# Kernel tuning notes

Measured on AMD Instinct MI355X. Metric: run time of the kernel, lower is better.

Reference implementation:

```python
import jax, jax.numpy as jnp
import numpy as np

N = 4096
IN_F = 512
OUT_F = 256
HEADS = 4
HEAD_DIM = OUT_F // HEADS


def setup_inputs() -> dict:
    key = jax.random.key(0)
    k_feat, k_adj, k_w, k_a = jax.random.split(key, 4)
    features = jax.random.normal(k_feat, (N, IN_F), dtype=jnp.float32)
    adj_matrix = jax.random.uniform(k_adj, (N, N), dtype=jnp.float32)
    # xavier-uniform-ish init scaled small
    W = jax.random.normal(k_w, (OUT_F, IN_F), dtype=jnp.float32) * (1.0 / np.sqrt(IN_F))
    a = jax.random.normal(k_a, (HEADS, 2 * HEAD_DIM), dtype=jnp.float32) * 0.1
    bias = jnp.zeros((OUT_F,), dtype=jnp.float32)
    return {"features": features, "adj_matrix": adj_matrix, "W": W, "a": a, "bias": bias}


def reference(features, adj_matrix, W, a, bias):
    n = features.shape[0]
    h = features @ W.T                      # [N, OUT_F]
    hh = h.reshape(n, HEADS, HEAD_DIM)      # [N, H, D]
    # e[i,j,h] = leaky_relu(<h_i, a[:, :D]> + <h_j, a[:, D:]>) -- additive decomposition
    e_src = jnp.einsum('nhd,hd->nh', hh, a[:, :HEAD_DIM])   # [N, H]
    e_dst = jnp.einsum('nhd,hd->nh', hh, a[:, HEAD_DIM:])   # [N, H]
    e = e_src[:, None, :] + e_dst[None, :, :]               # [N, N, H]
    e = jnp.where(e >= 0, e, 0.2 * e)                       # leaky_relu(0.2)
    mask = adj_matrix[:, :, None] > 0.1                     # [N, N, 1]
    e = jnp.where(mask, e, -jnp.inf)
    attention = jax.nn.softmax(e, axis=1)                   # softmax over j
    attention = jnp.nan_to_num(attention, nan=0.0)          # fully-masked rows -> 0
    attention_mean = attention.mean(axis=2)                 # [N, N]
    h_out = attention_mean @ h + bias                       # [N, OUT_F]
    return h_out
```

## Files before the change

### kernel.cpp

```cpp
#include <hip/hip_runtime.h>
#include <math.h>

#define NN      4096
#define INF_    512
#define OUTF    256
#define NHEAD   4
#define HDIM    64
#define KSPLIT  8

typedef __attribute__((ext_vector_type(8))) short  short8x;
typedef __attribute__((ext_vector_type(4))) float  float4x;
typedef __attribute__((ext_vector_type(2))) float  float2x;

__device__ __forceinline__ unsigned short f2bf(float x) {
    union { float f; unsigned int u; } c; c.f = x;
    unsigned int r = (c.u + 0x7FFFu + ((c.u >> 16) & 1u)) >> 16;
    return (unsigned short)r;
}
__device__ __forceinline__ unsigned int cvtpk_bf16(float lo, float hi) {
    unsigned int r;
    asm("v_cvt_pk_bf16_f32 %0, %1, %2" : "=v"(r) : "v"(lo), "v"(hi));
    return r;
}
__device__ __forceinline__ float2x bf2up(unsigned int u) {
    union { unsigned int x; float f; } lo, hi;
    lo.x = u << 16; hi.x = u & 0xFFFF0000u;
    float2x r; r[0] = lo.f; r[1] = hi.f; return r;
}
__device__ __forceinline__ float2x max2(float2x a, float2x b) {
    float2x r; r[0] = fmaxf(a[0], b[0]); r[1] = fmaxf(a[1], b[1]); return r;
}

__global__ __launch_bounds__(256) void k_cast(const float* __restrict__ feat,
                                              const float* __restrict__ W,
                                              const float* __restrict__ bias,
                                              unsigned short* __restrict__ featb,
                                              unsigned short* __restrict__ Wb,
                                              float* __restrict__ out) {
    const int b = blockIdx.x;
    const int tid = threadIdx.x;
    if (b >= 2176) {
        int idx = (b - 2176) * 1024 + tid * 4;
        float4x bv = *(const float4x*)(bias + ((tid * 4) & 255));
        *(float4x*)(out + idx) = bv;
        return;
    }
    const float* src;
    unsigned short* dst;
    int idx;
    if (b < 2048) { src = feat; dst = featb; idx = b * 1024 + tid * 4; }
    else          { src = W;    dst = Wb;    idx = (b - 2048) * 1024 + tid * 4; }
    float4x v = *(const float4x*)(src + idx);
    ushort4 u;
    u.x = f2bf(v[0]); u.y = f2bf(v[1]); u.z = f2bf(v[2]); u.w = f2bf(v[3]);
    *(ushort4*)(dst + idx) = u;
}

__global__ __launch_bounds__(256) void k_hedge(const unsigned short* __restrict__ featb,
                                               const unsigned short* __restrict__ Wb,
                                               const float* __restrict__ a,
                                               unsigned short* __restrict__ hT,
                                               float* __restrict__ es,
                                               unsigned short* __restrict__ Bt,
                                               unsigned short* __restrict__ Dt) {
    __shared__ __align__(16) unsigned short lds_f[32 * 40];
    __shared__ __align__(16) unsigned short lds_w[256 * 40];
    const int tid  = threadIdx.x;
    const int w    = tid >> 6;
    const int lane = tid & 63;
    const int lidx = lane & 15;
    const int quad = lane >> 4;
    const int i0   = blockIdx.x * 32;
    const int srf  = tid >> 3;
    const int skf  = (tid & 7) * 4;
    const int srw  = tid >> 2;
    const int skw  = (tid & 3) * 8;

    float4x acc[2][4];
    #pragma unroll
    for (int p = 0; p < 2; ++p)
        #pragma unroll
        for (int q = 0; q < 4; ++q)
            acc[p][q] = (float4x){0.f, 0.f, 0.f, 0.f};

    for (int kt = 0; kt < INF_; kt += 32) {
        __syncthreads();
        *(ushort4*)&lds_f[srf * 40 + skf] = *(const ushort4*)&featb[(size_t)(i0 + srf) * INF_ + kt + skf];
        #pragma unroll
        for (int itr = 0; itr < 4; ++itr) {
            int n = itr * 64 + srw;
            *(ushort4*)&lds_w[n * 40 + skw]     = *(const ushort4*)&Wb[(size_t)n * INF_ + kt + skw];
            *(ushort4*)&lds_w[n * 40 + skw + 4] = *(const ushort4*)&Wb[(size_t)n * INF_ + kt + skw + 4];
        }
        __syncthreads();
        short8x af[2], bw[4];
        #pragma unroll
        for (int t = 0; t < 2; ++t)
            af[t] = *(const short8x*)&lds_f[(t * 16 + lidx) * 40 + quad * 8];
        #pragma unroll
        for (int t = 0; t < 4; ++t)
            bw[t] = *(const short8x*)&lds_w[(w * 64 + t * 16 + lidx) * 40 + quad * 8];
        #pragma unroll
        for (int it = 0; it < 2; ++it)
            #pragma unroll
            for (int nt = 0; nt < 4; ++nt)
                acc[it][nt] = __builtin_amdgcn_mfma_f32_16x16x32_bf16(
                    af[it], bw[nt], acc[it][nt], 0, 0, 0);
    }
    #pragma unroll
    for (int it = 0; it < 2; ++it)
        #pragma unroll
        for (int nt = 0; nt < 4; ++nt) {
            int col = w * 64 + nt * 16 + lidx;
            int m0r = i0 + it * 16 + quad * 4;
            uint2 u;
            u.x = cvtpk_bf16(acc[it][nt][0], acc[it][nt][1]);
            u.y = cvtpk_bf16(acc[it][nt][2], acc[it][nt][3]);
            *(uint2*)&hT[(size_t)col * NN + m0r] = u;
        }
    float asrc[4], adst[4];
    #pragma unroll
    for (int nt = 0; nt < 4; ++nt) {
        asrc[nt] = a[w * 2 * HDIM + nt * 16 + lidx];
        adst[nt] = a[w * 2 * HDIM + HDIM + nt * 16 + lidx];
    }
    #pragma unroll
    for (int it = 0; it < 2; ++it)
        #pragma unroll
        for (int r = 0; r < 4; ++r) {
            float s = 0.f, d = 0.f;
            #pragma unroll
            for (int nt = 0; nt < 4; ++nt) {
                s += acc[it][nt][r] * asrc[nt];
                d += acc[it][nt][r] * adst[nt];
            }
            #pragma unroll
            for (int off = 1; off < 16; off <<= 1) {
                s += __shfl_xor(s, off);
                d += __shfl_xor(d, off);
            }
            if (lidx == 0) {
                int row = i0 + it * 16 + quad * 4 + r;
                es[row * NHEAD + w] = s;
                Bt[row * NHEAD + w] = f2bf(__expf(d));
                Dt[row * NHEAD + w] = f2bf(__expf(0.2f * d));
            }
        }
}

__global__ __launch_bounds__(256) void k_attn(const float* __restrict__ adj,
                                              const float* __restrict__ es,
                                              const unsigned short* __restrict__ Bt,
                                              const unsigned short* __restrict__ Dt,
                                              unsigned short* __restrict__ attn) {
    __shared__ float red[4][4];
    __shared__ float cfs[4];
    const int tid = threadIdx.x;
    const int wv  = tid >> 6;
    const int lane = tid & 63;
    const int i = blockIdx.x;

    const float4x esv = ((const float4x*)es)[i];
    float2x A01, A23, C01, C23;
    A01[0] = __expf(esv[0]); A01[1] = __expf(esv[1]);
    A23[0] = __expf(esv[2]); A23[1] = __expf(esv[3]);
    C01[0] = __expf(0.2f * esv[0]); C01[1] = __expf(0.2f * esv[1]);
    C23[0] = __expf(0.2f * esv[2]); C23[1] = __expf(0.2f * esv[3]);

    const float4x* arow4 = (const float4x*)(adj + (size_t)i * NN);
    const uint4* B4 = (const uint4*)Bt;
    const uint4* D4 = (const uint4*)Dt;

    float2x m01[4][4], m23[4][4];
    float2x den01 = (float2x){0.f, 0.f};
    float2x den23 = (float2x){0.f, 0.f};
    #pragma unroll
    for (int t = 0; t < 4; ++t) {
        int jv = t * 256 + tid;
        float4x av = arow4[jv];
        uint4 bu0 = B4[jv * 2], bu1 = B4[jv * 2 + 1];
        uint4 du0 = D4[jv * 2], du1 = D4[jv * 2 + 1];
        unsigned int bwv[8] = {bu0.x, bu0.y, bu0.z, bu0.w, bu1.x, bu1.y, bu1.z, bu1.w};
        unsigned int dwv[8] = {du0.x, du0.y, du0.z, du0.w, du1.x, du1.y, du1.z, du1.w};
        #pragma unroll
        for (int u = 0; u < 4; ++u) {
            float2x b01 = bf2up(bwv[u * 2]);
            float2x b23 = bf2up(bwv[u * 2 + 1]);
            float2x d01 = bf2up(dwv[u * 2]);
            float2x d23 = bf2up(dwv[u * 2 + 1]);
            float mf = (av[u] > 0.1f) ? 1.f : 0.f;
            float2x mf2; mf2[0] = mf; mf2[1] = mf;
            m01[t][u] = mf2 * max2(A01 * b01, C01 * d01);
            m23[t][u] = mf2 * max2(A23 * b23, C23 * d23);
            den01 += m01[t][u];
            den23 += m23[t][u];
        }
    }
    float dh[4] = {den01[0], den01[1], den23[0], den23[1]};
    #pragma unroll
    for (int off = 1; off < 64; off <<= 1) {
        #pragma unroll
        for (int h = 0; h < 4; ++h)
            dh[h] += __shfl_xor(dh[h], off);
    }
    if (lane == 0) {
        #pragma unroll
        for (int h = 0; h < 4; ++h) red[wv][h] = dh[h];
    }
    __syncthreads();
    if (tid < 4)
        cfs[tid] = red[0][tid] + red[1][tid] + red[2][tid] + red[3][tid];
    __syncthreads();
    float sc[4];
    #pragma unroll
    for (int h = 0; h < 4; ++h) {
        float den = cfs[h];
        sc[h] = den > 0.f ? 0.25f / den : 0.f;
    }

    unsigned short* orow = attn + (size_t)i * NN;
    #pragma unroll
    for (int t = 0; t < 4; ++t) {
        int jv = t * 256 + tid;
        float pv[4];
        #pragma unroll
        for (int u = 0; u < 4; ++u) {
            pv[u] = sc[0] * m01[t][u][0] + sc[1] * m01[t][u][1]
                  + sc[2] * m23[t][u][0] + sc[3] * m23[t][u][1];
        }
        uint2 o;
        o.x = cvtpk_bf16(pv[0], pv[1]);
        o.y = cvtpk_bf16(pv[2], pv[3]);
        *(uint2*)&orow[jv * 4] = o;
    }
}

__global__ __launch_bounds__(256) void k_out_gemm(const unsigned short* __restrict__ attn,
                                                  const unsigned short* __restrict__ hT,
                                                  float* __restrict__ out) {
    __shared__ __align__(16) unsigned short lds_a[32 * 72];
    __shared__ __align__(16) unsigned short lds_h[256 * 72];
    const int tid  = threadIdx.x;
    const int w    = tid >> 6;
    const int lane = tid & 63;
    const int lidx = lane & 15;
    const int quad = lane >> 4;
    const int i0    = blockIdx.x * 32;
    const int kbase = blockIdx.y * (NN / KSPLIT);
    const int sr   = tid >> 3;
    const int sc   = (tid & 7) * 8;

    float4x acc[2][4];
    #pragma unroll
    for (int p = 0; p < 2; ++p)
        #pragma unroll
        for (int q = 0; q < 4; ++q)
            acc[p][q] = (float4x){0.f, 0.f, 0.f, 0.f};

    short8x pa;
    short8x ph[8];
    pa = *(const short8x*)&attn[(size_t)(i0 + sr) * NN + kbase + sc];
    #pragma unroll
    for (int p = 0; p < 8; ++p)
        ph[p] = *(const short8x*)&hT[(size_t)(p * 32 + sr) * NN + kbase + sc];

    const int KSTEPS = (NN / KSPLIT) / 64;
    for (int ks = 0; ks < KSTEPS; ++ks) {
        __syncthreads();
        *(short8x*)&lds_a[sr * 72 + sc] = pa;
        #pragma unroll
        for (int p = 0; p < 8; ++p)
            *(short8x*)&lds_h[(p * 32 + sr) * 72 + sc] = ph[p];
        __syncthreads();
        if (ks + 1 < KSTEPS) {
            const int ko = kbase + (ks + 1) * 64;
            pa = *(const short8x*)&attn[(size_t)(i0 + sr) * NN + ko + sc];
            #pragma unroll
            for (int p = 0; p < 8; ++p)
                ph[p] = *(const short8x*)&hT[(size_t)(p * 32 + sr) * NN + ko + sc];
        }
        #pragma unroll
        for (int kk = 0; kk < 2; ++kk) {
            short8x af[2], bfr[4];
            #pragma unroll
            for (int it = 0; it < 2; ++it)
                af[it]  = *(const short8x*)&lds_a[(it * 16 + lidx) * 72 + kk * 32 + quad * 8];
            #pragma unroll
            for (int nt = 0; nt < 4; ++nt)
                bfr[nt] = *(const short8x*)&lds_h[(w * 64 + nt * 16 + lidx) * 72 + kk * 32 + quad * 8];
            #pragma unroll
            for (int it = 0; it < 2; ++it)
                #pragma unroll
                for (int nt = 0; nt < 4; ++nt)
                    acc[it][nt] = __builtin_amdgcn_mfma_f32_16x16x32_bf16(
                        af[it], bfr[nt], acc[it][nt], 0, 0, 0);
        }
    }
    #pragma unroll
    for (int it = 0; it < 2; ++it)
        #pragma unroll
        for (int nt = 0; nt < 4; ++nt)
            #pragma unroll
            for (int rr = 0; rr < 4; ++rr) {
                int row = i0 + it * 16 + quad * 4 + rr;
                int col = w * 64 + nt * 16 + lidx;
                unsafeAtomicAdd(&out[(size_t)row * OUTF + col], acc[it][nt][rr]);
            }
}

extern "C" void kernel_launch(void* const* d_in, const int* in_sizes, int n_in,
                              void* d_out, int out_size, void* d_ws, size_t ws_size,
                              hipStream_t stream) {
    const float* feat = (const float*)d_in[0];
    const float* adj  = (const float*)d_in[1];
    const float* W    = (const float*)d_in[2];
    const float* a    = (const float*)d_in[3];
    const float* bias = (const float*)d_in[4];
    float* out = (float*)d_out;

    char* ws = (char*)d_ws;
    float*          es    = (float*)(ws + 0);
    unsigned short* Btb   = (unsigned short*)(ws + (64u << 10));
    unsigned short* Dtb   = (unsigned short*)(ws + (96u << 10));
    unsigned short* hT    = (unsigned short*)(ws + (256u << 10));
    unsigned short* attn  = (unsigned short*)(ws + (2560u << 10));
    unsigned short* featb = (unsigned short*)(ws + (2560u << 10));
    unsigned short* Wb    = (unsigned short*)(ws + (6656u << 10));

    k_cast      <<<3200,              256, 0, stream>>>(feat, W, bias, featb, Wb, out);
    k_hedge     <<<128,               256, 0, stream>>>(featb, Wb, a, hT, es, Btb, Dtb);
    k_attn      <<<NN,                256, 0, stream>>>(adj, es, Btb, Dtb, attn);
    k_out_gemm  <<<dim3(128, KSPLIT), 256, 0, stream>>>(attn, hT, out);
}
```

Before: 172.2 us.

## Fuse attention-probability computation into output GEMM, split denominator pass

The attention kernel now only computes per-row softmax denominators and stores scaled per-head coefficients. The output GEMM recomputes the bf16 attention probabilities on the fly from adj, Bt and Dt instead of reading a materialized 32MB bf16 attention matrix. This removes the attention write and re-read, but reads adj twice (once per kernel) and adds exp-free elementwise work inside the GEMM loop. KSPLIT is also halved to 4, which reduces atomic traffic and gives longer K loops per block.

```diff
diff --git a/kernel.cpp b/kernel.cpp
--- a/kernel.cpp
+++ b/kernel.cpp
@@ -6,7 +6,7 @@
 #define OUTF    256
 #define NHEAD   4
 #define HDIM    64
-#define KSPLIT  8
+#define KSPLIT  4
 
 typedef __attribute__((ext_vector_type(8))) short  short8x;
 typedef __attribute__((ext_vector_type(4))) float  float4x;
@@ -148,11 +148,11 @@
         }
 }
 
-__global__ __launch_bounds__(256) void k_attn(const float* __restrict__ adj,
-                                              const float* __restrict__ es,
-                                              const unsigned short* __restrict__ Bt,
-                                              const unsigned short* __restrict__ Dt,
-                                              unsigned short* __restrict__ attn) {
+__global__ __launch_bounds__(256) void k_den(const float* __restrict__ adj,
+                                             const float* __restrict__ es,
+                                             const unsigned short* __restrict__ Bt,
+                                             const unsigned short* __restrict__ Dt,
+                                             float* __restrict__ cden) {
     __shared__ float red[4][4];
     __shared__ float cfs[4];
     const int tid = threadIdx.x;
@@ -171,7 +171,6 @@
     const uint4* B4 = (const uint4*)Bt;
     const uint4* D4 = (const uint4*)Dt;
 
-    float2x m01[4][4], m23[4][4];
     float2x den01 = (float2x){0.f, 0.f};
     float2x den23 = (float2x){0.f, 0.f};
     #pragma unroll
@@ -190,10 +189,8 @@
             float2x d23 = bf2up(dwv[u * 2 + 1]);
             float mf = (av[u] > 0.1f) ? 1.f : 0.f;
             float2x mf2; mf2[0] = mf; mf2[1] = mf;
-            m01[t][u] = mf2 * max2(A01 * b01, C01 * d01);
-            m23[t][u] = mf2 * max2(A23 * b23, C23 * d23);
-            den01 += m01[t][u];
-            den23 += m23[t][u];
+            den01 += mf2 * max2(A01 * b01, C01 * d01);
+            den23 += mf2 * max2(A23 * b23, C23 * d23);
         }
     }
     float dh[4] = {den01[0], den01[1], den23[0], den23[1]};
@@ -211,34 +208,29 @@
     if (tid < 4)
         cfs[tid] = red[0][tid] + red[1][tid] + red[2][tid] + red[3][tid];
     __syncthreads();
-    float sc[4];
-    #pragma unroll
-    for (int h = 0; h < 4; ++h) {
-        float den = cfs[h];
-        sc[h] = den > 0.f ? 0.25f / den : 0.f;
-    }
-
-    unsigned short* orow = attn + (size_t)i * NN;
-    #pragma unroll
-    for (int t = 0; t < 4; ++t) {
-        int jv = t * 256 + tid;
-        float pv[4];
-        #pragma unroll
-        for (int u = 0; u < 4; ++u) {
-            pv[u] = sc[0] * m01[t][u][0] + sc[1] * m01[t][u][1]
-                  + sc[2] * m23[t][u][0] + sc[3] * m23[t][u][1];
-        }
-        uint2 o;
-        o.x = cvtpk_bf16(pv[0], pv[1]);
-        o.y = cvtpk_bf16(pv[2], pv[3]);
-        *(uint2*)&orow[jv * 4] = o;
-    }
-}
-
-__global__ __launch_bounds__(256) void k_out_gemm(const unsigned short* __restrict__ attn,
-                                                  const unsigned short* __restrict__ hT,
-                                                  float* __restrict__ out) {
-    __shared__ __align__(16) unsigned short lds_a[32 * 72];
+    if (tid == 0) {
+        float A[4] = {A01[0], A01[1], A23[0], A23[1]};
+        float C[4] = {C01[0], C01[1], C23[0], C23[1]};
+        float4x cA, cC;
+        #pragma unroll
+        for (int h = 0; h < 4; ++h) {
+            float den = cfs[h];
+            float sc = den > 0.f ? 0.25f / den : 0.f;
+            cA[h] = A[h] * sc;
+            cC[h] = C[h] * sc;
+        }
+        ((float4x*)cden)[i * 2]     = cA;
+        ((float4x*)cden)[i * 2 + 1] = cC;
+    }
+}
+
+__global__ __launch_bounds__(256) void k_fused(const float* __restrict__ adj,
+                                               const float* __restrict__ cden,
+                                               const unsigned short* __restrict__ Bt,
+                                               const unsigned short* __restrict__ Dt,
+                                               const unsigned short* __restrict__ hT,
+                                               float* __restrict__ out) {
+    __shared__ __align__(16) unsigned short lds_p[32 * 72];
     __shared__ __align__(16) unsigned short lds_h[256 * 72];
     const int tid  = threadIdx.x;
     const int w    = tid >> 6;
@@ -248,7 +240,16 @@
     const int i0    = blockIdx.x * 32;
     const int kbase = blockIdx.y * (NN / KSPLIT);
     const int sr   = tid >> 3;
-    const int sc   = (tid & 7) * 8;
+    const int sc8  = (tid & 7) * 8;
+
+    const float4x cAv = ((const float4x*)cden)[(i0 + sr) * 2];
+    const float4x cCv = ((const float4x*)cden)[(i0 + sr) * 2 + 1];
+    float2x cA01, cA23, cC01, cC23;
+    cA01[0] = cAv[0]; cA01[1] = cAv[1]; cA23[0] = cAv[2]; cA23[1] = cAv[3];
+    cC01[0] = cCv[0]; cC01[1] = cCv[1]; cC23[0] = cCv[2]; cC23[1] = cCv[3];
+
+    const uint4* B4 = (const uint4*)Bt;
+    const uint4* D4 = (const uint4*)Dt;
 
     float4x acc[2][4];
     #pragma unroll
@@ -257,34 +258,69 @@
         for (int q = 0; q < 4; ++q)
             acc[p][q] = (float4x){0.f, 0.f, 0.f, 0.f};
 
-    short8x pa;
-    short8x ph[8];
-    pa = *(const short8x*)&attn[(size_t)(i0 + sr) * NN + kbase + sc];
-    #pragma unroll
-    for (int p = 0; p < 8; ++p)
-        ph[p] = *(const short8x*)&hT[(size_t)(p * 32 + sr) * NN + kbase + sc];
+    short8x pb[8];
+    short8x pp;
+
+    auto COMPP = [&](int ks) {
+        const int jb = kbase + ks * 64 + sc8;
+        float4x a0 = *(const float4x*)&adj[(size_t)(i0 + sr) * NN + jb];
+        float4x a1 = *(const float4x*)&adj[(size_t)(i0 + sr) * NN + jb + 4];
+        uint4 bu0 = B4[jb >> 1], bu1 = B4[(jb >> 1) + 1];
+        uint4 bu2 = B4[(jb >> 1) + 2], bu3 = B4[(jb >> 1) + 3];
+        uint4 du0 = D4[jb >> 1], du1 = D4[(jb >> 1) + 1];
+        uint4 du2 = D4[(jb >> 1) + 2], du3 = D4[(jb >> 1) + 3];
+        unsigned int bw[16] = {bu0.x, bu0.y, bu0.z, bu0.w, bu1.x, bu1.y, bu1.z, bu1.w,
+                               bu2.x, bu2.y, bu2.z, bu2.w, bu3.x, bu3.y, bu3.z, bu3.w};
+        unsigned int dw[16] = {du0.x, du0.y, du0.z, du0.w, du1.x, du1.y, du1.z, du1.w,
+                               du2.x, du2.y, du2.z, du2.w, du3.x, du3.y, du3.z, du3.w};
+        float pv[8];
+        #pragma unroll
+        for (int jj = 0; jj < 8; ++jj) {
+            float2x b01 = bf2up(bw[jj * 2]);
+            float2x b23 = bf2up(bw[jj * 2 + 1]);
+            float2x d01 = bf2up(dw[jj * 2]);
+            float2x d23 = bf2up(dw[jj * 2 + 1]);
+            float2x t01 = max2(cA01 * b01, cC01 * d01);
+            float2x t23 = max2(cA23 * b23, cC23 * d23);
+            float av = (jj < 4) ? a0[jj] : a1[jj - 4];
+            float s = (t01[0] + t01[1]) + (t23[0] + t23[1]);
+            pv[jj] = (av > 0.1f) ? s : 0.f;
+        }
+        union { short8x s; unsigned int u[4]; } pk;
+        pk.u[0] = cvtpk_bf16(pv[0], pv[1]);
+        pk.u[1] = cvtpk_bf16(pv[2], pv[3]);
+        pk.u[2] = cvtpk_bf16(pv[4], pv[5]);
+        pk.u[3] = cvtpk_bf16(pv[6], pv[7]);
+        pp = pk.s;
+    };
+    auto LOADB = [&](int ks) {
+        const int ko = kbase + ks * 64;
+        #pragma unroll
+        for (int p = 0; p < 8; ++p)
+            pb[p] = *(const short8x*)&hT[(size_t)(p * 32 + sr) * NN + ko + sc8];
+    };
+
+    LOADB(0);
+    COMPP(0);
 
     const int KSTEPS = (NN / KSPLIT) / 64;
     for (int ks = 0; ks < KSTEPS; ++ks) {
         __syncthreads();
-        *(short8x*)&lds_a[sr * 72 + sc] = pa;
+        *(short8x*)&lds_p[sr * 72 + sc8] = pp;
         #pragma unroll
         for (int p = 0; p < 8; ++p)
-            *(short8x*)&lds_h[(p * 32 + sr) * 72 + sc] = ph[p];
+            *(short8x*)&lds_h[(p * 32 + sr) * 72 + sc8] = pb[p];
         __syncthreads();
         if (ks + 1 < KSTEPS) {
-            const int ko = kbase + (ks + 1) * 64;
-            pa = *(const short8x*)&attn[(size_t)(i0 + sr) * NN + ko + sc];
-            #pragma unroll
-            for (int p = 0; p < 8; ++p)
-                ph[p] = *(const short8x*)&hT[(size_t)(p * 32 + sr) * NN + ko + sc];
+            LOADB(ks + 1);
+            COMPP(ks + 1);
         }
         #pragma unroll
         for (int kk = 0; kk < 2; ++kk) {
             short8x af[2], bfr[4];
             #pragma unroll
             for (int it = 0; it < 2; ++it)
-                af[it]  = *(const short8x*)&lds_a[(it * 16 + lidx) * 72 + kk * 32 + quad * 8];
+                af[it]  = *(const short8x*)&lds_p[(it * 16 + lidx) * 72 + kk * 32 + quad * 8];
             #pragma unroll
             for (int nt = 0; nt < 4; ++nt)
                 bfr[nt] = *(const short8x*)&lds_h[(w * 64 + nt * 16 + lidx) * 72 + kk * 32 + quad * 8];
@@ -322,13 +358,13 @@
     float*          es    = (float*)(ws + 0);
     unsigned short* Btb   = (unsigned short*)(ws + (64u << 10));
     unsigned short* Dtb   = (unsigned short*)(ws + (96u << 10));
+    float*          cden  = (float*)(ws + (128u << 10));
     unsigned short* hT    = (unsigned short*)(ws + (256u << 10));
-    unsigned short* attn  = (unsigned short*)(ws + (2560u << 10));
     unsigned short* featb = (unsigned short*)(ws + (2560u << 10));
     unsigned short* Wb    = (unsigned short*)(ws + (6656u << 10));
 
-    k_cast      <<<3200,              256, 0, stream>>>(feat, W, bias, featb, Wb, out);
-    k_hedge     <<<128,               256, 0, stream>>>(featb, Wb, a, hT, es, Btb, Dtb);
-    k_attn      <<<NN,                256, 0, stream>>>(adj, es, Btb, Dtb, attn);
-    k_out_gemm  <<<dim3(128, KSPLIT), 256, 0, stream>>>(attn, hT, out);
-}
+    k_cast <<<3200,              256, 0, stream>>>(feat, W, bias, featb, Wb, out);
+    k_hedge<<<128,               256, 0, stream>>>(featb, Wb, a, hT, es, Btb, Dtb);
+    k_den  <<<NN,                256, 0, stream>>>(adj, es, Btb, Dtb, cden);
+    k_fused<<<dim3(128, KSPLIT), 256, 0, stream>>>(adj, cden, Btb, Dtb, hT, out);
+}
```

Result: slower. 177.2 us (+2.9%).

## Fuse fp32-to-bf16 cast and bias init into projection GEMM kernel

Applied to the files above, without the earlier changes.

Drops the separate cast kernel. The projection kernel now loads fp32 features and W directly, converts them to bf16 as it stages them into LDS, and writes the bias into the output rows it owns. The row tile shrinks from 32 to 16 and the K step grows from 32 to 64, so the grid doubles to 256 blocks. This removes one launch and the bf16 round trip through global memory. In exchange, each block re-reads and re-converts the whole fp32 W matrix, which adds L2 traffic.

```diff
diff --git a/kernel.cpp b/kernel.cpp
--- a/kernel.cpp
+++ b/kernel.cpp
@@ -31,93 +31,88 @@
     float2x r; r[0] = fmaxf(a[0], b[0]); r[1] = fmaxf(a[1], b[1]); return r;
 }
 
-__global__ __launch_bounds__(256) void k_cast(const float* __restrict__ feat,
-                                              const float* __restrict__ W,
-                                              const float* __restrict__ bias,
-                                              unsigned short* __restrict__ featb,
-                                              unsigned short* __restrict__ Wb,
-                                              float* __restrict__ out) {
-    const int b = blockIdx.x;
-    const int tid = threadIdx.x;
-    if (b >= 2176) {
-        int idx = (b - 2176) * 1024 + tid * 4;
-        float4x bv = *(const float4x*)(bias + ((tid * 4) & 255));
-        *(float4x*)(out + idx) = bv;
-        return;
-    }
-    const float* src;
-    unsigned short* dst;
-    int idx;
-    if (b < 2048) { src = feat; dst = featb; idx = b * 1024 + tid * 4; }
-    else          { src = W;    dst = Wb;    idx = (b - 2048) * 1024 + tid * 4; }
-    float4x v = *(const float4x*)(src + idx);
-    ushort4 u;
-    u.x = f2bf(v[0]); u.y = f2bf(v[1]); u.z = f2bf(v[2]); u.w = f2bf(v[3]);
-    *(ushort4*)(dst + idx) = u;
-}
-
-__global__ __launch_bounds__(256) void k_hedge(const unsigned short* __restrict__ featb,
-                                               const unsigned short* __restrict__ Wb,
+__global__ __launch_bounds__(256) void k_hedge(const float* __restrict__ feat,
+                                               const float* __restrict__ W,
                                                const float* __restrict__ a,
+                                               const float* __restrict__ bias,
                                                unsigned short* __restrict__ hT,
                                                float* __restrict__ es,
                                                unsigned short* __restrict__ Bt,
-                                               unsigned short* __restrict__ Dt) {
-    __shared__ __align__(16) unsigned short lds_f[32 * 40];
-    __shared__ __align__(16) unsigned short lds_w[256 * 40];
+                                               unsigned short* __restrict__ Dt,
+                                               float* __restrict__ out) {
+    __shared__ __align__(16) unsigned short lds_f[16 * 72];
+    __shared__ __align__(16) unsigned short lds_w[256 * 72];
     const int tid  = threadIdx.x;
     const int w    = tid >> 6;
     const int lane = tid & 63;
     const int lidx = lane & 15;
     const int quad = lane >> 4;
-    const int i0   = blockIdx.x * 32;
-    const int srf  = tid >> 3;
-    const int skf  = (tid & 7) * 4;
-    const int srw  = tid >> 2;
-    const int skw  = (tid & 3) * 8;
-
-    float4x acc[2][4];
-    #pragma unroll
-    for (int p = 0; p < 2; ++p)
-        #pragma unroll
-        for (int q = 0; q < 4; ++q)
-            acc[p][q] = (float4x){0.f, 0.f, 0.f, 0.f};
-
-    for (int kt = 0; kt < INF_; kt += 32) {
+    const int i0   = blockIdx.x * 16;
+
+    {
+        float4x bv = *(const float4x*)(bias + ((tid * 4) & 255));
+        float* ob = out + (size_t)i0 * OUTF;
+        #pragma unroll
+        for (int itr = 0; itr < 4; ++itr)
+            *(float4x*)(ob + itr * 1024 + tid * 4) = bv;
+    }
+
+    const int fr = tid >> 4;
+    const int fc = (tid & 15) * 4;
+    const int wr = tid >> 2;
+    const int wc = (tid & 3) * 16;
+
+    float4x acc[4];
+    #pragma unroll
+    for (int q = 0; q < 4; ++q)
+        acc[q] = (float4x){0.f, 0.f, 0.f, 0.f};
+
+    for (int kt = 0; kt < INF_; kt += 64) {
         __syncthreads();
-        *(ushort4*)&lds_f[srf * 40 + skf] = *(const ushort4*)&featb[(size_t)(i0 + srf) * INF_ + kt + skf];
-        #pragma unroll
-        for (int itr = 0; itr < 4; ++itr) {
-            int n = itr * 64 + srw;
-            *(ushort4*)&lds_w[n * 40 + skw]     = *(const ushort4*)&Wb[(size_t)n * INF_ + kt + skw];
-            *(ushort4*)&lds_w[n * 40 + skw + 4] = *(const ushort4*)&Wb[(size_t)n * INF_ + kt + skw + 4];
+        {
+            float4x v = *(const float4x*)&feat[(size_t)(i0 + fr) * INF_ + kt + fc];
+            uint2 u;
+            u.x = cvtpk_bf16(v[0], v[1]);
+            u.y = cvtpk_bf16(v[2], v[3]);
+            *(uint2*)&lds_f[fr * 72 + fc] = u;
+        }
+        #pragma unroll
+        for (int p = 0; p < 4; ++p) {
+            int row = p * 64 + wr;
+            const float* src = &W[(size_t)row * INF_ + kt + wc];
+            float4x v0 = *(const float4x*)(src);
+            float4x v1 = *(const float4x*)(src + 4);
+            float4x v2 = *(const float4x*)(src + 8);
+            float4x v3 = *(const float4x*)(src + 12);
+            union { short8x s; unsigned int u[4]; } p0, p1;
+            p0.u[0] = cvtpk_bf16(v0[0], v0[1]); p0.u[1] = cvtpk_bf16(v0[2], v0[3]);
+            p0.u[2] = cvtpk_bf16(v1[0], v1[1]); p0.u[3] = cvtpk_bf16(v1[2], v1[3]);
+            p1.u[0] = cvtpk_bf16(v2[0], v2[1]); p1.u[1] = cvtpk_bf16(v2[2], v2[3]);
+            p1.u[2] = cvtpk_bf16(v3[0], v3[1]); p1.u[3] = cvtpk_bf16(v3[2], v3[3]);
+            *(short8x*)&lds_w[row * 72 + wc]     = p0.s;
+            *(short8x*)&lds_w[row * 72 + wc + 8] = p1.s;
         }
         __syncthreads();
-        short8x af[2], bw[4];
-        #pragma unroll
-        for (int t = 0; t < 2; ++t)
-            af[t] = *(const short8x*)&lds_f[(t * 16 + lidx) * 40 + quad * 8];
-        #pragma unroll
-        for (int t = 0; t < 4; ++t)
-            bw[t] = *(const short8x*)&lds_w[(w * 64 + t * 16 + lidx) * 40 + quad * 8];
-        #pragma unroll
-        for (int it = 0; it < 2; ++it)
+        #pragma unroll
+        for (int kk = 0; kk < 2; ++kk) {
+            short8x af = *(const short8x*)&lds_f[lidx * 72 + kk * 32 + quad * 8];
+            short8x bw[4];
             #pragma unroll
             for (int nt = 0; nt < 4; ++nt)
-                acc[it][nt] = __builtin_amdgcn_mfma_f32_16x16x32_bf16(
-                    af[it], bw[nt], acc[it][nt], 0, 0, 0);
-    }
-    #pragma unroll
-    for (int it = 0; it < 2; ++it)
-        #pragma unroll
-        for (int nt = 0; nt < 4; ++nt) {
-            int col = w * 64 + nt * 16 + lidx;
-            int m0r = i0 + it * 16 + quad * 4;
-            uint2 u;
-            u.x = cvtpk_bf16(acc[it][nt][0], acc[it][nt][1]);
-            u.y = cvtpk_bf16(acc[it][nt][2], acc[it][nt][3]);
-            *(uint2*)&hT[(size_t)col * NN + m0r] = u;
-        }
+                bw[nt] = *(const short8x*)&lds_w[(w * 64 + nt * 16 + lidx) * 72 + kk * 32 + quad * 8];
+            #pragma unroll
+            for (int nt = 0; nt < 4; ++nt)
+                acc[nt] = __builtin_amdgcn_mfma_f32_16x16x32_bf16(af, bw[nt], acc[nt], 0, 0, 0);
+        }
+    }
+    #pragma unroll
+    for (int nt = 0; nt < 4; ++nt) {
+        int col = w * 64 + nt * 16 + lidx;
+        uint2 u;
+        u.x = cvtpk_bf16(acc[nt][0], acc[nt][1]);
+        u.y = cvtpk_bf16(acc[nt][2], acc[nt][3]);
+        *(uint2*)&hT[(size_t)col * NN + i0 + quad * 4] = u;
+    }
     float asrc[4], adst[4];
     #pragma unroll
     for (int nt = 0; nt < 4; ++nt) {
@@ -125,27 +120,25 @@
         adst[nt] = a[w * 2 * HDIM + HDIM + nt * 16 + lidx];
     }
     #pragma unroll
-    for (int it = 0; it < 2; ++it)
-        #pragma unroll
-        for (int r = 0; r < 4; ++r) {
-            float s = 0.f, d = 0.f;
-            #pragma unroll
-            for (int nt = 0; nt < 4; ++nt) {
-                s += acc[it][nt][r] * asrc[nt];
-                d += acc[it][nt][r] * adst[nt];
-            }
-            #pragma unroll
-            for (int off = 1; off < 16; off <<= 1) {
-                s += __shfl_xor(s, off);
-                d += __shfl_xor(d, off);
-            }
-            if (lidx == 0) {
-                int row = i0 + it * 16 + quad * 4 + r;
-                es[row * NHEAD + w] = s;
-                Bt[row * NHEAD + w] = f2bf(__expf(d));
-                Dt[row * NHEAD + w] = f2bf(__expf(0.2f * d));
-            }
-        }
+    for (int r = 0; r < 4; ++r) {
+        float s = 0.f, d = 0.f;
+        #pragma unroll
+        for (int nt = 0; nt < 4; ++nt) {
+            s += acc[nt][r] * asrc[nt];
+            d += acc[nt][r] * adst[nt];
+        }
+        #pragma unroll
+        for (int off = 1; off < 16; off <<= 1) {
+            s += __shfl_xor(s, off);
+            d += __shfl_xor(d, off);
+        }
+        if (lidx == 0) {
+            int row = i0 + quad * 4 + r;
+            es[row * NHEAD + w] = s;
+            Bt[row * NHEAD + w] = f2bf(__expf(d));
+            Dt[row * NHEAD + w] = f2bf(__expf(0.2f * d));
+        }
+    }
 }
 
 __global__ __launch_bounds__(256) void k_attn(const float* __restrict__ adj,
@@ -324,11 +317,8 @@
     unsigned short* Dtb   = (unsigned short*)(ws + (96u << 10));
     unsigned short* hT    = (unsigned short*)(ws + (256u << 10));
     unsigned short* attn  = (unsigned short*)(ws + (2560u << 10));
-    unsigned short* featb = (unsigned short*)(ws + (2560u << 10));
-    unsigned short* Wb    = (unsigned short*)(ws + (6656u << 10));
-
-    k_cast      <<<3200,              256, 0, stream>>>(feat, W, bias, featb, Wb, out);
-    k_hedge     <<<128,               256, 0, stream>>>(featb, Wb, a, hT, es, Btb, Dtb);
-    k_attn      <<<NN,                256, 0, stream>>>(adj, es, Btb, Dtb, attn);
-    k_out_gemm  <<<dim3(128, KSPLIT), 256, 0, stream>>>(attn, hT, out);
-}
+
+    k_hedge    <<<256,               256, 0, stream>>>(feat, W, a, bias, hT, es, Btb, Dtb, out);
+    k_attn     <<<NN,                256, 0, stream>>>(adj, es, Btb, Dtb, attn);
+    k_out_gemm <<<dim3(128, KSPLIT), 256, 0, stream>>>(attn, hT, out);
+}
```

Result: no change. 170.9 us (-0.8%).
